# Kernel tuning notes

Hardware: AMD Instinct MI355X
Metric: run time of the kernel (lower is better)

The kernel has to match this reference:

```python
import jax, jax.numpy as jnp
import numpy as np

BLOCK = 4  # block_size from init_kwargs


def space_to_channel_3d(x, b):
    # Faithful translation of SpaceToChannel_3d.forward (torch split/stack/permute chain).
    B, C, W, H, D = x.shape
    y = x.transpose(0, 2, 3, 4, 1)                      # (B, W, H, D, C)
    y = y.reshape(B, W, H, D // b, b, C)                # split depth into D//b chunks of b
    y = y.transpose(0, 3, 1, 2, 4, 5)                   # (B, D//b, W, H, b, C)
    y = y.reshape(B, D // b, W // b, H // b, C * b * b * b)  # per-chunk row-major reshape
    y = y.transpose(0, 2, 3, 1, 4)                      # (B, W//b, H//b, D//b, C*b^3)
    return y.transpose(0, 4, 1, 2, 3)                   # (B, C*b^3, W//b, H//b, D//b)


def channel_to_space_3d(x, b):
    # Faithful translation of ChannelToSpace_3d.forward.
    B, Cd, wd, hd, dd = x.shape
    b3 = b * b * b
    Cs = Cd // b3
    y = x.transpose(0, 2, 3, 4, 1)                      # (B, wd, hd, dd, Cd)
    y = y.reshape(B, wd, hd, dd, b * b, b, Cs)          # split b^3 dim into b^2 chunks of b
    y = y.transpose(0, 4, 1, 2, 3, 5, 6)                # (B, b^2, wd, hd, dd, b, Cs)
    y = y.reshape(B, b * b, wd, hd, dd * b, Cs)         # merge (dd, b) per chunk
    y = y.transpose(0, 2, 1, 3, 4, 5)                   # (B, wd, b^2, hd, dd*b, Cs)
    y = y.reshape(B, wd * b, hd * b, dd * b, Cs)        # row-major merge of (wd, b^2, hd)
    return y.transpose(0, 4, 1, 2, 3)                   # (B, Cs, wd*b, hd*b, dd*b)


def setup_inputs() -> dict:
    key = jax.random.key(0)
    k1, k2 = jax.random.split(key)
    x = jax.random.normal(k1, (4, 32, 64, 64, 64), dtype=jnp.float32)
    gamma = jax.random.normal(k2, (1,), dtype=jnp.float32)
    return {"x": x, "gamma": gamma}


def reference(x, gamma):
    b = BLOCK
    y = space_to_channel_3d(x, b)                       # (B, C*b^3, w, h, d)
    B, C, w, h, d = y.shape
    q = y.reshape(B, C, w * h * d)                      # (B, C', N)
    # channel-wise attention: energy (B, C', C')
    energy = jnp.einsum('bcn,ben->bce', q, q)
    energy_new = jnp.max(energy, axis=-1, keepdims=True) - energy
    attention = jax.nn.softmax(energy_new, axis=-1)
    out = jnp.einsum('bce,ben->bcn', attention, q)      # (B, C', N)
    out = out.reshape(B, C, w, h, d)
    out = gamma * out + y
    return channel_to_space_3d(out, b)
```

## Files before the change

### kernel.cpp

```cpp
#include <hip/hip_runtime.h>

typedef _Float16 f16;
typedef __attribute__((ext_vector_type(8))) _Float16 f16x8;
typedef __attribute__((ext_vector_type(4))) float f32x4;

#define CCH 2048
#define NSP 4096
#define NB  4

__device__ __forceinline__ void gld16(const void* g, void* l) {
  __builtin_amdgcn_global_load_lds(
      (const __attribute__((address_space(1))) void*)g,
      (__attribute__((address_space(3))) void*)l, 16, 0, 0);
}

__global__ void pack_kernel(const float* __restrict__ x, f16* __restrict__ qh,
                            f16* __restrict__ ql, int b0) {
  int gid = blockIdx.x * 256 + threadIdx.x;
  int n = gid & (NSP - 1);
  int t = gid >> 12;
  int c = t & 31; t >>= 5;
  int r = t & 15; int ib = t >> 4;
  int wc = n >> 8, hc = (n >> 4) & 15, dc = n & 15;
  int w = wc * 4 + (hc >> 2);
  int h = (hc & 3) * 16 + r;
  int b = b0 + ib;
  const f32x4 v = *(const f32x4*)(x + ((((size_t)b * 32 + c) * 64 + w) * 64 + h) * 64 + dc * 4);
#pragma unroll
  for (int bd = 0; bd < 4; ++bd) {
    int cc = r * 128 + bd * 32 + c;
    size_t o = ((size_t)ib * CCH + cc) * NSP + n;
    float val = v[bd];
    f16 hi = (f16)val;
    qh[o] = hi;
    ql[o] = (f16)(val - (float)hi);
  }
}

__global__ void transpose_kernel(const f16* __restrict__ qh, f16* __restrict__ qhT) {
  int ib = blockIdx.z;
  int j0 = blockIdx.x * 64, n0 = blockIdx.y * 64;
  __shared__ f16 tile[64][72];
  int t = threadIdx.x;
  int r = t >> 3;
  int cb = (t & 7) * 8;
#pragma unroll
  for (int half = 0; half < 2; ++half) {
    int rr = r + half * 32;
    f16x8 v = *(const f16x8*)(qh + ((size_t)ib * CCH + j0 + rr) * NSP + n0 + cb);
    *(f16x8*)&tile[rr][cb] = v;
  }
  __syncthreads();
#pragma unroll
  for (int half = 0; half < 2; ++half) {
    int rr = r + half * 32;
    f16x8 o;
#pragma unroll
    for (int u = 0; u < 8; ++u) o[u] = tile[cb + u][rr];
    *(f16x8*)(qhT + ((size_t)ib * NSP + n0 + rr) * CCH + j0 + cb) = o;
  }
}

__global__ __launch_bounds__(256) void gemm1_kernel(const f16* __restrict__ qh,
                                                    const f16* __restrict__ ql,
                                                    float* __restrict__ energy,
                                                    int ksplit) {
  int ib = blockIdx.z;
  int nwg = gridDim.x;
  int cpx = nwg >> 3;
  int bx = blockIdx.x;
  int tri = (bx & 7) * cpx + (bx >> 3);
  int ks = 0;
  if (ksplit == 2) { ks = tri >= 136; tri -= ks * 136; }
  int rem = tri, bi = 0, span = 16;
  while (rem >= span) { rem -= span; ++bi; --span; }
  int bj = bi + rem;
  int i0 = bi * 128, j0 = bj * 128;
  int kbeg = ks * 2048;
  int kend = (ksplit == 2) ? kbeg + 2048 : NSP;
  float* eout = energy + ((size_t)(ks * gridDim.z + ib)) * CCH * CCH;

  __shared__ f16 Lds[2][4][128 * 32];
  int tid = threadIdx.x;
  int lane = tid & 63, wv = tid >> 6;
  int l15 = lane & 15, quad = lane >> 4;
  int wr = (wv >> 1) * 64, wcol = (wv & 1) * 64;
  int swz = (l15 >> 1) & 3;
  int kbs = (lane & 3) ^ ((lane >> 3) & 3);

  const f16* srcA = (wv & 1) ? ql : qh;
  int rbase = (wv < 2) ? i0 : j0;
  const f16* gsrc = srcA + ((size_t)ib * CCH + rbase) * NSP
                    + (size_t)(lane >> 2) * NSP + kbs * 8;

  auto stage = [&](int buf, int kk) {
    f16* ld = &Lds[buf][wv][0];
#pragma unroll
    for (int t = 0; t < 8; ++t)
      gld16(gsrc + (size_t)(t * 16) * NSP + kk, ld + t * 512);
  };

  const f32x4 vzero = {0.f, 0.f, 0.f, 0.f};
  f32x4 acc[4][4];
#pragma unroll
  for (int a = 0; a < 4; ++a)
#pragma unroll
    for (int bq = 0; bq < 4; ++bq) acc[a][bq] = vzero;

  int nk = (kend - kbeg) >> 5;
  stage(0, kbeg);
  __syncthreads();
  for (int it = 0; it < nk; ++it) {
    int cur = it & 1;
    if (it + 1 < nk) stage(cur ^ 1, kbeg + ((it + 1) << 5));
    f16x8 ah[4], al[4], bh[4], bl[4];
#pragma unroll
    for (int mt = 0; mt < 4; ++mt) {
      int row = wr + mt * 16 + l15;
      ah[mt] = *(const f16x8*)&Lds[cur][0][row * 32 + ((quad ^ swz) * 8)];
      al[mt] = *(const f16x8*)&Lds[cur][1][row * 32 + ((quad ^ swz) * 8)];
    }
#pragma unroll
    for (int nt = 0; nt < 4; ++nt) {
      int col = wcol + nt * 16 + l15;
      bh[nt] = *(const f16x8*)&Lds[cur][2][col * 32 + ((quad ^ swz) * 8)];
      bl[nt] = *(const f16x8*)&Lds[cur][3][col * 32 + ((quad ^ swz) * 8)];
    }
    __builtin_amdgcn_s_setprio(1);
#pragma unroll
    for (int mt = 0; mt < 4; ++mt)
#pragma unroll
      for (int nt = 0; nt < 4; ++nt) {
        acc[mt][nt] = __builtin_amdgcn_mfma_f32_16x16x32_f16(ah[mt], bh[nt], acc[mt][nt], 0, 0, 0);
        acc[mt][nt] = __builtin_amdgcn_mfma_f32_16x16x32_f16(ah[mt], bl[nt], acc[mt][nt], 0, 0, 0);
        acc[mt][nt] = __builtin_amdgcn_mfma_f32_16x16x32_f16(al[mt], bh[nt], acc[mt][nt], 0, 0, 0);
      }
    __builtin_amdgcn_s_setprio(0);
    __syncthreads();
  }
  bool diag = (bi == bj);
#pragma unroll
  for (int mt = 0; mt < 4; ++mt)
#pragma unroll
    for (int nt = 0; nt < 4; ++nt)
#pragma unroll
      for (int rg = 0; rg < 4; ++rg) {
        int row = i0 + wr + mt * 16 + quad * 4 + rg;
        int col = j0 + wcol + nt * 16 + l15;
        float v = acc[mt][nt][rg];
        eout[(size_t)row * CCH + col] = v;
        if (!diag) eout[(size_t)col * CCH + row] = v;
      }
}

__global__ void softmax_kernel(const float* __restrict__ e0, const float* __restrict__ e1,
                               int two, const float* __restrict__ gamma_p,
                               f16* __restrict__ attn) {
  int i = blockIdx.x, ib = blockIdx.y;
  const float* r0 = e0 + ((size_t)ib * CCH + i) * CCH;
  const float* r1 = e1 + ((size_t)ib * CCH + i) * CCH;
  f16* arow = attn + ((size_t)ib * CCH + i) * CCH;
  int t = threadIdx.x;
  f32x4 v0 = *(const f32x4*)(r0 + t * 8);
  f32x4 v1 = *(const f32x4*)(r0 + t * 8 + 4);
  if (two) {
    f32x4 u0 = *(const f32x4*)(r1 + t * 8);
    f32x4 u1 = *(const f32x4*)(r1 + t * 8 + 4);
#pragma unroll
    for (int u = 0; u < 4; ++u) { v0[u] += u0[u]; v1[u] += u1[u]; }
  }
  float m = v0[0];
#pragma unroll
  for (int u = 1; u < 4; ++u) m = fminf(m, v0[u]);
#pragma unroll
  for (int u = 0; u < 4; ++u) m = fminf(m, v1[u]);
#pragma unroll
  for (int off = 32; off > 0; off >>= 1) m = fminf(m, __shfl_xor(m, off));
  __shared__ float redA[4], redB[4];
  if ((t & 63) == 0) redA[t >> 6] = m;
  __syncthreads();
  m = fminf(fminf(redA[0], redA[1]), fminf(redA[2], redA[3]));
  float e[8], s = 0.f;
#pragma unroll
  for (int u = 0; u < 4; ++u) { e[u] = __expf(m - v0[u]); s += e[u]; }
#pragma unroll
  for (int u = 0; u < 4; ++u) { e[4 + u] = __expf(m - v1[u]); s += e[4 + u]; }
#pragma unroll
  for (int off = 32; off > 0; off >>= 1) s += __shfl_xor(s, off);
  if ((t & 63) == 0) redB[t >> 6] = s;
  __syncthreads();
  s = redB[0] + redB[1] + redB[2] + redB[3];
  float gamma = *gamma_p;
  float ginv = gamma / s;
  int du = i - t * 8;
  f16x8 o;
#pragma unroll
  for (int u = 0; u < 8; ++u) {
    float v = e[u] * ginv;
    if (u == du) v += 1.0f;
    o[u] = (f16)v;
  }
  *(f16x8*)(arow + t * 8) = o;
}

__global__ __launch_bounds__(256) void gemm2_kernel(const f16* __restrict__ attn,
                                                    const f16* __restrict__ qhT,
                                                    float* __restrict__ out, int b0) {
  int ib = blockIdx.z;
  int lin = blockIdx.x + gridDim.x * blockIdx.y;
  int nwg = gridDim.x * gridDim.y;
  int cpx = nwg >> 3;
  int lin2 = (lin & 7) * cpx + (lin >> 3);
  int i0 = (lin2 & 15) * 128;
  int n0 = (lin2 >> 4) * 128;
  __shared__ f16 Lds[2][2][2][128 * 32];
  int tid = threadIdx.x;
  int lane = tid & 63, wv = tid >> 6;
  int l15 = lane & 15, quad = lane >> 4;
  int wr = (wv >> 1) * 64, wcol = (wv & 1) * 64;
  int swz = (l15 >> 1) & 3;
  int kbs = (lane & 3) ^ ((lane >> 3) & 3);

  const f16* asrc = attn + ((size_t)ib * CCH + i0) * CCH;
  const f16* bsrc = qhT + ((size_t)ib * NSP + n0) * CCH;
  int rowoff = (wv & 1) * 64;
  int tidx = wv >> 1;
  const f16* gbase = (wv < 2) ? asrc : bsrc;
  const f16* gsrc = gbase + (size_t)(rowoff + (lane >> 2)) * CCH + kbs * 8;

  auto stage = [&](int buf, int kk) {
#pragma unroll
    for (int kh = 0; kh < 2; ++kh)
#pragma unroll
      for (int t = 0; t < 4; ++t)
        gld16(gsrc + (size_t)(t * 16) * CCH + kk + kh * 32,
              &Lds[buf][tidx][kh][(rowoff + t * 16) * 32]);
  };

  const f32x4 vzero = {0.f, 0.f, 0.f, 0.f};
  f32x4 acc[4][4];
#pragma unroll
  for (int a = 0; a < 4; ++a)
#pragma unroll
    for (int bq = 0; bq < 4; ++bq) acc[a][bq] = vzero;

  stage(0, 0);
  __syncthreads();
  for (int it = 0; it < CCH / 64; ++it) {
    int cur = it & 1;
    if (it + 1 < CCH / 64) stage(cur ^ 1, (it + 1) << 6);
    f16x8 af[4][2], bf[4][2];
#pragma unroll
    for (int kh = 0; kh < 2; ++kh) {
#pragma unroll
      for (int mt = 0; mt < 4; ++mt)
        af[mt][kh] = *(const f16x8*)&Lds[cur][0][kh][(wr + mt * 16 + l15) * 32 + ((quad ^ swz) * 8)];
#pragma unroll
      for (int nt = 0; nt < 4; ++nt)
        bf[nt][kh] = *(const f16x8*)&Lds[cur][1][kh][(wcol + nt * 16 + l15) * 32 + ((quad ^ swz) * 8)];
    }
    __builtin_amdgcn_s_setprio(1);
#pragma unroll
    for (int kh = 0; kh < 2; ++kh)
#pragma unroll
      for (int mt = 0; mt < 4; ++mt)
#pragma unroll
        for (int nt = 0; nt < 4; ++nt)
          acc[mt][nt] = __builtin_amdgcn_mfma_f32_16x16x32_f16(af[mt][kh], bf[nt][kh], acc[mt][nt], 0, 0, 0);
    __builtin_amdgcn_s_setprio(0);
    __syncthreads();
  }

  float* eld = (float*)&Lds[0][0][0][0];
#pragma unroll
  for (int mt = 0; mt < 4; ++mt) {
    int f = (wr >> 5) + (mt >> 1);
    int gb = (mt & 1) * 16 + quad * 4;
#pragma unroll
    for (int nt = 0; nt < 4; ++nt) {
      int jh = (wcol >> 4) + nt;
#pragma unroll
      for (int rg = 0; rg < 4; ++rg)
        eld[(gb + rg) * 512 + jh * 64 + l15 * 4 + f] = acc[mt][nt][rg];
    }
  }
  __syncthreads();
  int b = b0 + ib;
  int e = i0 >> 7;
  int iw = n0 >> 8;
  int W = iw * 4 + (e >> 2);
  int H0 = (e & 3) * 16 + ((n0 >> 4) & 15);
#pragma unroll
  for (int u = 0; u < 8; ++u) {
    int g = wv * 8 + u;
    size_t goff = ((((size_t)b * 32 + g) * 64 + W) * 4096) + (size_t)H0 * 64;
#pragma unroll
    for (int hv = 0; hv < 2; ++hv) {
      int fo = hv * 256 + lane * 4;
      *(f32x4*)(out + goff + fo) = *(const f32x4*)&eld[g * 512 + fo];
    }
  }
}

extern "C" void kernel_launch(void* const* d_in, const int* in_sizes, int n_in,
                              void* d_out, int out_size, void* d_ws, size_t ws_size,
                              hipStream_t stream) {
  const float* x = (const float*)d_in[0];
  const float* gamma = (const float*)d_in[1];
  float* out = (float*)d_out;

  const size_t szQ = (size_t)CCH * NSP;
  const size_t szE = (size_t)CCH * CCH;

  const size_t pbSplit = szQ * 2 * 3 + szE * 4 * 2 + szE * 2;
  const size_t pbNoSplit = szQ * 2 * 3 + szE * 4 + szE * 2;

  int ksplit, nb;
  if (ws_size >= (size_t)NB * pbSplit) { ksplit = 2; nb = NB; }
  else if (ws_size >= (size_t)NB * pbNoSplit) { ksplit = 1; nb = NB; }
  else { ksplit = 1; nb = 1; }

  char* p = (char*)d_ws;
  f16* qh = (f16*)p;   p += (size_t)nb * szQ * 2;
  f16* ql = (f16*)p;   p += (size_t)nb * szQ * 2;
  f16* qhT = (f16*)p;  p += (size_t)nb * szQ * 2;
  float* energy = (float*)p; p += (size_t)nb * szE * 4 * ksplit;
  f16* attn = (f16*)p;
  const float* e1 = (ksplit == 2) ? (energy + (size_t)nb * szE) : energy;

  for (int b0 = 0; b0 < NB; b0 += nb) {
    pack_kernel<<<nb * 8192, 256, 0, stream>>>(x, qh, ql, b0);
    transpose_kernel<<<dim3(32, 64, nb), 256, 0, stream>>>(qh, qhT);
    gemm1_kernel<<<dim3(136 * ksplit, 1, nb), 256, 0, stream>>>(qh, ql, energy, ksplit);
    softmax_kernel<<<dim3(CCH, nb), 256, 0, stream>>>(energy, e1, ksplit - 1, gamma, attn);
    gemm2_kernel<<<dim3(16, 32, nb), 256, 0, stream>>>(attn, qhT, out, b0);
  }
}
```

Baseline: 750.7 us.

## Use 4-slot LDS pipeline with vmcnt waits and drop gemm1 K-split

Both GEMMs now use a four-slot LDS ring with three stages in flight. Each iteration waits on an explicit vmcnt count and a raw s_barrier instead of using double buffering with __syncthreads. gemm1 splits its three hi/lo products into separate phases that each stream one operand pair, and the K-split path is removed. This cuts the number of grid blocks for gemm1 from 272 to 136 per batch and drops the second energy buffer and its sum in softmax. The deeper prefetch is meant to hide global load latency, but gemm1 now has fewer workgroups, which reduces occupancy across the CUs.

```diff
diff --git a/kernel.cpp b/kernel.cpp
--- a/kernel.cpp
+++ b/kernel.cpp
@@ -7,6 +7,11 @@
 #define CCH 2048
 #define NSP 4096
 #define NB  4
+
+#define VMCNT8 asm volatile("s_waitcnt vmcnt(8)" ::: "memory")
+#define VMCNT4 asm volatile("s_waitcnt vmcnt(4)" ::: "memory")
+#define VMCNT0 asm volatile("s_waitcnt vmcnt(0)" ::: "memory")
+#define CFENCE asm volatile("" ::: "memory")
 
 __device__ __forceinline__ void gld16(const void* g, void* l) {
   __builtin_amdgcn_global_load_lds(
@@ -63,24 +68,17 @@
 
 __global__ __launch_bounds__(256) void gemm1_kernel(const f16* __restrict__ qh,
                                                     const f16* __restrict__ ql,
-                                                    float* __restrict__ energy,
-                                                    int ksplit) {
+                                                    float* __restrict__ energy) {
   int ib = blockIdx.z;
-  int nwg = gridDim.x;
-  int cpx = nwg >> 3;
   int bx = blockIdx.x;
-  int tri = (bx & 7) * cpx + (bx >> 3);
-  int ks = 0;
-  if (ksplit == 2) { ks = tri >= 136; tri -= ks * 136; }
+  int tri = (bx & 7) * 17 + (bx >> 3);
   int rem = tri, bi = 0, span = 16;
   while (rem >= span) { rem -= span; ++bi; --span; }
   int bj = bi + rem;
   int i0 = bi * 128, j0 = bj * 128;
-  int kbeg = ks * 2048;
-  int kend = (ksplit == 2) ? kbeg + 2048 : NSP;
-  float* eout = energy + ((size_t)(ks * gridDim.z + ib)) * CCH * CCH;
-
-  __shared__ f16 Lds[2][4][128 * 32];
+  float* eout = energy + (size_t)ib * CCH * CCH;
+
+  __shared__ f16 Lds[4][2][128 * 32];
   int tid = threadIdx.x;
   int lane = tid & 63, wv = tid >> 6;
   int l15 = lane & 15, quad = lane >> 4;
@@ -88,16 +86,20 @@
   int swz = (l15 >> 1) & 3;
   int kbs = (lane & 3) ^ ((lane >> 3) & 3);
 
-  const f16* srcA = (wv & 1) ? ql : qh;
-  int rbase = (wv < 2) ? i0 : j0;
-  const f16* gsrc = srcA + ((size_t)ib * CCH + rbase) * NSP
-                    + (size_t)(lane >> 2) * NSP + kbs * 8;
-
-  auto stage = [&](int buf, int kk) {
-    f16* ld = &Lds[buf][wv][0];
-#pragma unroll
-    for (int t = 0; t < 8; ++t)
-      gld16(gsrc + (size_t)(t * 16) * NSP + kk, ld + t * 512);
+  int arr = wv >> 1, rh = wv & 1;
+  int rbase = arr ? j0 : i0;
+  size_t rowoff = ((size_t)ib * CCH + rbase + rh * 64 + (lane >> 2)) * NSP + kbs * 8;
+  const f16* gqh = qh + rowoff;
+  const f16* gql = ql + rowoff;
+
+  auto stage = [&](int slot, int q) {
+    const f16* src = arr ? (((q >> 7) == 1) ? gql : gqh)
+                         : (((q >> 7) == 2) ? gql : gqh);
+    int kk = (q & 127) << 5;
+#pragma unroll
+    for (int t = 0; t < 4; ++t)
+      gld16(src + (size_t)(t * 16) * NSP + kk,
+            &Lds[slot][arr][(rh * 64 + t * 16) * 32]);
   };
 
   const f32x4 vzero = {0.f, 0.f, 0.f, 0.f};
@@ -107,36 +109,31 @@
 #pragma unroll
     for (int bq = 0; bq < 4; ++bq) acc[a][bq] = vzero;
 
-  int nk = (kend - kbeg) >> 5;
-  stage(0, kbeg);
-  __syncthreads();
-  for (int it = 0; it < nk; ++it) {
-    int cur = it & 1;
-    if (it + 1 < nk) stage(cur ^ 1, kbeg + ((it + 1) << 5));
-    f16x8 ah[4], al[4], bh[4], bl[4];
-#pragma unroll
-    for (int mt = 0; mt < 4; ++mt) {
-      int row = wr + mt * 16 + l15;
-      ah[mt] = *(const f16x8*)&Lds[cur][0][row * 32 + ((quad ^ swz) * 8)];
-      al[mt] = *(const f16x8*)&Lds[cur][1][row * 32 + ((quad ^ swz) * 8)];
-    }
-#pragma unroll
-    for (int nt = 0; nt < 4; ++nt) {
-      int col = wcol + nt * 16 + l15;
-      bh[nt] = *(const f16x8*)&Lds[cur][2][col * 32 + ((quad ^ swz) * 8)];
-      bl[nt] = *(const f16x8*)&Lds[cur][3][col * 32 + ((quad ^ swz) * 8)];
-    }
+  const int NP = 3 * (NSP / 32);
+  stage(0, 0); stage(1, 1); stage(2, 2);
+  for (int p = 0; p < NP; ++p) {
+    int remp = NP - 1 - p;
+    if (remp >= 2) { VMCNT8; } else if (remp == 1) { VMCNT4; } else { VMCNT0; }
+    __builtin_amdgcn_s_barrier();
+    CFENCE;
+    if (p + 3 < NP) stage((p + 3) & 3, p + 3);
+    int s = p & 3;
+    const f16* As = &Lds[s][0][0];
+    const f16* Bs = &Lds[s][1][0];
+    f16x8 ah[4], bh[4];
+#pragma unroll
+    for (int mt = 0; mt < 4; ++mt)
+      ah[mt] = *(const f16x8*)&As[(wr + mt * 16 + l15) * 32 + ((quad ^ swz) * 8)];
+#pragma unroll
+    for (int nt = 0; nt < 4; ++nt)
+      bh[nt] = *(const f16x8*)&Bs[(wcol + nt * 16 + l15) * 32 + ((quad ^ swz) * 8)];
     __builtin_amdgcn_s_setprio(1);
 #pragma unroll
     for (int mt = 0; mt < 4; ++mt)
 #pragma unroll
-      for (int nt = 0; nt < 4; ++nt) {
+      for (int nt = 0; nt < 4; ++nt)
         acc[mt][nt] = __builtin_amdgcn_mfma_f32_16x16x32_f16(ah[mt], bh[nt], acc[mt][nt], 0, 0, 0);
-        acc[mt][nt] = __builtin_amdgcn_mfma_f32_16x16x32_f16(ah[mt], bl[nt], acc[mt][nt], 0, 0, 0);
-        acc[mt][nt] = __builtin_amdgcn_mfma_f32_16x16x32_f16(al[mt], bh[nt], acc[mt][nt], 0, 0, 0);
-      }
     __builtin_amdgcn_s_setprio(0);
-    __syncthreads();
   }
   bool diag = (bi == bj);
 #pragma unroll
@@ -153,22 +150,15 @@
       }
 }
 
-__global__ void softmax_kernel(const float* __restrict__ e0, const float* __restrict__ e1,
-                               int two, const float* __restrict__ gamma_p,
+__global__ void softmax_kernel(const float* __restrict__ e0,
+                               const float* __restrict__ gamma_p,
                                f16* __restrict__ attn) {
   int i = blockIdx.x, ib = blockIdx.y;
   const float* r0 = e0 + ((size_t)ib * CCH + i) * CCH;
-  const float* r1 = e1 + ((size_t)ib * CCH + i) * CCH;
   f16* arow = attn + ((size_t)ib * CCH + i) * CCH;
   int t = threadIdx.x;
   f32x4 v0 = *(const f32x4*)(r0 + t * 8);
   f32x4 v1 = *(const f32x4*)(r0 + t * 8 + 4);
-  if (two) {
-    f32x4 u0 = *(const f32x4*)(r1 + t * 8);
-    f32x4 u1 = *(const f32x4*)(r1 + t * 8 + 4);
-#pragma unroll
-    for (int u = 0; u < 4; ++u) { v0[u] += u0[u]; v1[u] += u1[u]; }
-  }
   float m = v0[0];
 #pragma unroll
   for (int u = 1; u < 4; ++u) m = fminf(m, v0[u]);
@@ -213,7 +203,7 @@
   int lin2 = (lin & 7) * cpx + (lin >> 3);
   int i0 = (lin2 & 15) * 128;
   int n0 = (lin2 >> 4) * 128;
-  __shared__ f16 Lds[2][2][2][128 * 32];
+  __shared__ f16 Lds[4][2][128 * 32];
   int tid = threadIdx.x;
   int lane = tid & 63, wv = tid >> 6;
   int l15 = lane & 15, quad = lane >> 4;
@@ -221,20 +211,16 @@
   int swz = (l15 >> 1) & 3;
   int kbs = (lane & 3) ^ ((lane >> 3) & 3);
 
-  const f16* asrc = attn + ((size_t)ib * CCH + i0) * CCH;
-  const f16* bsrc = qhT + ((size_t)ib * NSP + n0) * CCH;
-  int rowoff = (wv & 1) * 64;
-  int tidx = wv >> 1;
-  const f16* gbase = (wv < 2) ? asrc : bsrc;
-  const f16* gsrc = gbase + (size_t)(rowoff + (lane >> 2)) * CCH + kbs * 8;
-
-  auto stage = [&](int buf, int kk) {
-#pragma unroll
-    for (int kh = 0; kh < 2; ++kh)
-#pragma unroll
-      for (int t = 0; t < 4; ++t)
-        gld16(gsrc + (size_t)(t * 16) * CCH + kk + kh * 32,
-              &Lds[buf][tidx][kh][(rowoff + t * 16) * 32]);
+  int arr = wv >> 1, rh = wv & 1;
+  const f16* gbase = arr ? (qhT + ((size_t)ib * NSP + n0) * CCH)
+                         : (attn + ((size_t)ib * CCH + i0) * CCH);
+  const f16* gsrc = gbase + (size_t)(rh * 64 + (lane >> 2)) * CCH + kbs * 8;
+
+  auto stage = [&](int slot, int kk) {
+#pragma unroll
+    for (int t = 0; t < 4; ++t)
+      gld16(gsrc + (size_t)(t * 16) * CCH + kk,
+            &Lds[slot][arr][(rh * 64 + t * 16) * 32]);
   };
 
   const f32x4 vzero = {0.f, 0.f, 0.f, 0.f};
@@ -244,34 +230,35 @@
 #pragma unroll
     for (int bq = 0; bq < 4; ++bq) acc[a][bq] = vzero;
 
-  stage(0, 0);
-  __syncthreads();
-  for (int it = 0; it < CCH / 64; ++it) {
-    int cur = it & 1;
-    if (it + 1 < CCH / 64) stage(cur ^ 1, (it + 1) << 6);
-    f16x8 af[4][2], bf[4][2];
-#pragma unroll
-    for (int kh = 0; kh < 2; ++kh) {
-#pragma unroll
-      for (int mt = 0; mt < 4; ++mt)
-        af[mt][kh] = *(const f16x8*)&Lds[cur][0][kh][(wr + mt * 16 + l15) * 32 + ((quad ^ swz) * 8)];
+  const int NP = CCH / 32;
+  stage(0, 0); stage(1, 32); stage(2, 64);
+  for (int p = 0; p < NP; ++p) {
+    int remp = NP - 1 - p;
+    if (remp >= 2) { VMCNT8; } else if (remp == 1) { VMCNT4; } else { VMCNT0; }
+    __builtin_amdgcn_s_barrier();
+    CFENCE;
+    if (p + 3 < NP) stage((p + 3) & 3, (p + 3) << 5);
+    int s = p & 3;
+    const f16* As = &Lds[s][0][0];
+    const f16* Bs = &Lds[s][1][0];
+    f16x8 af[4], bf[4];
+#pragma unroll
+    for (int mt = 0; mt < 4; ++mt)
+      af[mt] = *(const f16x8*)&As[(wr + mt * 16 + l15) * 32 + ((quad ^ swz) * 8)];
+#pragma unroll
+    for (int nt = 0; nt < 4; ++nt)
+      bf[nt] = *(const f16x8*)&Bs[(wcol + nt * 16 + l15) * 32 + ((quad ^ swz) * 8)];
+    __builtin_amdgcn_s_setprio(1);
+#pragma unroll
+    for (int mt = 0; mt < 4; ++mt)
 #pragma unroll
       for (int nt = 0; nt < 4; ++nt)
-        bf[nt][kh] = *(const f16x8*)&Lds[cur][1][kh][(wcol + nt * 16 + l15) * 32 + ((quad ^ swz) * 8)];
-    }
-    __builtin_amdgcn_s_setprio(1);
-#pragma unroll
-    for (int kh = 0; kh < 2; ++kh)
-#pragma unroll
-      for (int mt = 0; mt < 4; ++mt)
-#pragma unroll
-        for (int nt = 0; nt < 4; ++nt)
-          acc[mt][nt] = __builtin_amdgcn_mfma_f32_16x16x32_f16(af[mt][kh], bf[nt][kh], acc[mt][nt], 0, 0, 0);
+        acc[mt][nt] = __builtin_amdgcn_mfma_f32_16x16x32_f16(af[mt], bf[nt], acc[mt][nt], 0, 0, 0);
     __builtin_amdgcn_s_setprio(0);
-    __syncthreads();
-  }
-
-  float* eld = (float*)&Lds[0][0][0][0];
+  }
+
+  __syncthreads();
+  float* eld = (float*)&Lds[0][0][0];
 #pragma unroll
   for (int mt = 0; mt < 4; ++mt) {
     int f = (wr >> 5) + (mt >> 1);
@@ -312,27 +299,22 @@
   const size_t szQ = (size_t)CCH * NSP;
   const size_t szE = (size_t)CCH * CCH;
 
-  const size_t pbSplit = szQ * 2 * 3 + szE * 4 * 2 + szE * 2;
-  const size_t pbNoSplit = szQ * 2 * 3 + szE * 4 + szE * 2;
-
-  int ksplit, nb;
-  if (ws_size >= (size_t)NB * pbSplit) { ksplit = 2; nb = NB; }
-  else if (ws_size >= (size_t)NB * pbNoSplit) { ksplit = 1; nb = NB; }
-  else { ksplit = 1; nb = 1; }
+  const size_t pb = szQ * 2 * 3 + szE * 4 + szE * 2;
+
+  int nb = (ws_size >= (size_t)NB * pb) ? NB : 1;
 
   char* p = (char*)d_ws;
   f16* qh = (f16*)p;   p += (size_t)nb * szQ * 2;
   f16* ql = (f16*)p;   p += (size_t)nb * szQ * 2;
   f16* qhT = (f16*)p;  p += (size_t)nb * szQ * 2;
-  float* energy = (float*)p; p += (size_t)nb * szE * 4 * ksplit;
+  float* energy = (float*)p; p += (size_t)nb * szE * 4;
   f16* attn = (f16*)p;
-  const float* e1 = (ksplit == 2) ? (energy + (size_t)nb * szE) : energy;
 
   for (int b0 = 0; b0 < NB; b0 += nb) {
     pack_kernel<<<nb * 8192, 256, 0, stream>>>(x, qh, ql, b0);
     transpose_kernel<<<dim3(32, 64, nb), 256, 0, stream>>>(qh, qhT);
-    gemm1_kernel<<<dim3(136 * ksplit, 1, nb), 256, 0, stream>>>(qh, ql, energy, ksplit);
-    softmax_kernel<<<dim3(CCH, nb), 256, 0, stream>>>(energy, e1, ksplit - 1, gamma, attn);
+    gemm1_kernel<<<dim3(136, 1, nb), 256, 0, stream>>>(qh, ql, energy);
+    softmax_kernel<<<dim3(CCH, nb), 256, 0, stream>>>(energy, gamma, attn);
     gemm2_kernel<<<dim3(16, 32, nb), 256, 0, stream>>>(attn, qhT, out, b0);
   }
 }
```

After: 841.6 us. +12.1%, slower.

## Use 4-slot K=32 LDS ring with vmcnt waits in gemm2 pipeline

Applied to the files above, without the earlier changes.

Restructures the gemm2 main loop from a double-buffered K=64 scheme with a full __syncthreads per step into a four-slot ring of K=32 stages, keeping three stages of global-to-LDS loads in flight. Each step waits with explicit s_waitcnt vmcnt counts and a raw s_barrier instead of draining all outstanding loads. The goal is to hide global load latency behind MFMA work. In exchange it runs twice as many barriers with less MFMA work between them, and correctness now depends on the hand-counted vmcnt values matching the number of issued loads.

```diff
diff --git a/kernel.cpp b/kernel.cpp
--- a/kernel.cpp
+++ b/kernel.cpp
@@ -7,6 +7,11 @@
 #define CCH 2048
 #define NSP 4096
 #define NB  4
+
+#define VMCNT8 asm volatile("s_waitcnt vmcnt(8)" ::: "memory")
+#define VMCNT4 asm volatile("s_waitcnt vmcnt(4)" ::: "memory")
+#define VMCNT0 asm volatile("s_waitcnt vmcnt(0)" ::: "memory")
+#define CFENCE asm volatile("" ::: "memory")
 
 __device__ __forceinline__ void gld16(const void* g, void* l) {
   __builtin_amdgcn_global_load_lds(
@@ -213,7 +218,7 @@
   int lin2 = (lin & 7) * cpx + (lin >> 3);
   int i0 = (lin2 & 15) * 128;
   int n0 = (lin2 >> 4) * 128;
-  __shared__ f16 Lds[2][2][2][128 * 32];
+  __shared__ f16 Lds[4][2][128 * 32];
   int tid = threadIdx.x;
   int lane = tid & 63, wv = tid >> 6;
   int l15 = lane & 15, quad = lane >> 4;
@@ -221,20 +226,16 @@
   int swz = (l15 >> 1) & 3;
   int kbs = (lane & 3) ^ ((lane >> 3) & 3);
 
-  const f16* asrc = attn + ((size_t)ib * CCH + i0) * CCH;
-  const f16* bsrc = qhT + ((size_t)ib * NSP + n0) * CCH;
-  int rowoff = (wv & 1) * 64;
-  int tidx = wv >> 1;
-  const f16* gbase = (wv < 2) ? asrc : bsrc;
-  const f16* gsrc = gbase + (size_t)(rowoff + (lane >> 2)) * CCH + kbs * 8;
-
-  auto stage = [&](int buf, int kk) {
-#pragma unroll
-    for (int kh = 0; kh < 2; ++kh)
-#pragma unroll
-      for (int t = 0; t < 4; ++t)
-        gld16(gsrc + (size_t)(t * 16) * CCH + kk + kh * 32,
-              &Lds[buf][tidx][kh][(rowoff + t * 16) * 32]);
+  int arr = wv >> 1, rh = wv & 1;
+  const f16* gbase = arr ? (qhT + ((size_t)ib * NSP + n0) * CCH)
+                         : (attn + ((size_t)ib * CCH + i0) * CCH);
+  const f16* gsrc = gbase + (size_t)(rh * 64 + (lane >> 2)) * CCH + kbs * 8;
+
+  auto stage = [&](int slot, int kk) {
+#pragma unroll
+    for (int t = 0; t < 4; ++t)
+      gld16(gsrc + (size_t)(t * 16) * CCH + kk,
+            &Lds[slot][arr][(rh * 64 + t * 16) * 32]);
   };
 
   const f32x4 vzero = {0.f, 0.f, 0.f, 0.f};
@@ -244,34 +245,35 @@
 #pragma unroll
     for (int bq = 0; bq < 4; ++bq) acc[a][bq] = vzero;
 
-  stage(0, 0);
-  __syncthreads();
-  for (int it = 0; it < CCH / 64; ++it) {
-    int cur = it & 1;
-    if (it + 1 < CCH / 64) stage(cur ^ 1, (it + 1) << 6);
-    f16x8 af[4][2], bf[4][2];
-#pragma unroll
-    for (int kh = 0; kh < 2; ++kh) {
-#pragma unroll
-      for (int mt = 0; mt < 4; ++mt)
-        af[mt][kh] = *(const f16x8*)&Lds[cur][0][kh][(wr + mt * 16 + l15) * 32 + ((quad ^ swz) * 8)];
+  const int NP = CCH / 32;
+  stage(0, 0); stage(1, 32); stage(2, 64);
+  for (int p = 0; p < NP; ++p) {
+    int remp = NP - 1 - p;
+    if (remp >= 2) { VMCNT8; } else if (remp == 1) { VMCNT4; } else { VMCNT0; }
+    __builtin_amdgcn_s_barrier();
+    CFENCE;
+    if (p + 3 < NP) stage((p + 3) & 3, (p + 3) << 5);
+    int s = p & 3;
+    const f16* As = &Lds[s][0][0];
+    const f16* Bs = &Lds[s][1][0];
+    f16x8 af[4], bf[4];
+#pragma unroll
+    for (int mt = 0; mt < 4; ++mt)
+      af[mt] = *(const f16x8*)&As[(wr + mt * 16 + l15) * 32 + ((quad ^ swz) * 8)];
+#pragma unroll
+    for (int nt = 0; nt < 4; ++nt)
+      bf[nt] = *(const f16x8*)&Bs[(wcol + nt * 16 + l15) * 32 + ((quad ^ swz) * 8)];
+    __builtin_amdgcn_s_setprio(1);
+#pragma unroll
+    for (int mt = 0; mt < 4; ++mt)
 #pragma unroll
       for (int nt = 0; nt < 4; ++nt)
-        bf[nt][kh] = *(const f16x8*)&Lds[cur][1][kh][(wcol + nt * 16 + l15) * 32 + ((quad ^ swz) * 8)];
-    }
-    __builtin_amdgcn_s_setprio(1);
-#pragma unroll
-    for (int kh = 0; kh < 2; ++kh)
-#pragma unroll
-      for (int mt = 0; mt < 4; ++mt)
-#pragma unroll
-        for (int nt = 0; nt < 4; ++nt)
-          acc[mt][nt] = __builtin_amdgcn_mfma_f32_16x16x32_f16(af[mt][kh], bf[nt][kh], acc[mt][nt], 0, 0, 0);
+        acc[mt][nt] = __builtin_amdgcn_mfma_f32_16x16x32_f16(af[mt], bf[nt], acc[mt][nt], 0, 0, 0);
     __builtin_amdgcn_s_setprio(0);
-    __syncthreads();
-  }
-
-  float* eld = (float*)&Lds[0][0][0][0];
+  }
+
+  __syncthreads();
+  float* eld = (float*)&Lds[0][0][0];
 #pragma unroll
   for (int mt = 0; mt < 4; ++mt) {
     int f = (wr >> 5) + (mt >> 1);
```

After: 728.7 us. 1.03x faster.
